# Performance work log

Hardware: AMD Instinct MI355X
Metric: run time of the kernel (lower is better)

## Reference

```python
import jax, jax.numpy as jnp
import numpy as np
import math

B, S, D, H = 2, 2048, 2048, 16
HD = D // H  # 128
EPS = 1e-5


def setup_inputs() -> dict:
    key = jax.random.key(0)
    ks = jax.random.split(key, 8)
    s = 0.02
    return {
        "x": jax.random.normal(ks[0], (B, S, D), jnp.float32),
        "ln1_s": jnp.ones((D,), jnp.float32),
        "ln1_b": jnp.zeros((D,), jnp.float32),
        "Wq": jax.random.normal(ks[1], (D, D), jnp.float32) * s,
        "Wk": jax.random.normal(ks[2], (D, D), jnp.float32) * s,
        "Wv": jax.random.normal(ks[3], (D, D), jnp.float32) * s,
        "Wo": jax.random.normal(ks[4], (D, D), jnp.float32) * s,
        "bo": jnp.zeros((D,), jnp.float32),
        "ln2_s": jnp.ones((D,), jnp.float32),
        "ln2_b": jnp.zeros((D,), jnp.float32),
        "W1": jax.random.normal(ks[5], (D, 4 * D), jnp.float32) * s,
        "b1": jnp.zeros((4 * D,), jnp.float32),
        "W2": jax.random.normal(ks[6], (4 * D, D), jnp.float32) * s,
        "b2": jnp.zeros((D,), jnp.float32),
    }


def _layernorm(x, scale, shift):
    mean = jnp.mean(x, axis=-1, keepdims=True)
    var = jnp.var(x, axis=-1, keepdims=True)  # unbiased=False
    return scale * (x - mean) * jax.lax.rsqrt(var + EPS) + shift


def _gelu_tanh(x):
    c = math.sqrt(2.0 / math.pi)
    return 0.5 * x * (1.0 + jnp.tanh(c * (x + 0.044715 * x * x * x)))


def reference(x, ln1_s, ln1_b, Wq, Wk, Wv, Wo, bo, ln2_s, ln2_b, W1, b1, W2, b2):
    b, n, d = x.shape
    # --- pre-norm MHA ---
    xn = _layernorm(x, ln1_s, ln1_b)
    q = (xn @ Wq).reshape(b, n, H, HD)
    k = (xn @ Wk).reshape(b, n, H, HD)
    v = (xn @ Wv).reshape(b, n, H, HD)
    scores = jnp.einsum("bqhd,bkhd->bhqk", q, k) / math.sqrt(HD)
    causal = jnp.tril(jnp.ones((n, n), bool))  # True = keep
    scores = jnp.where(causal, scores, -jnp.inf)
    attn = jax.nn.softmax(scores, axis=-1)
    ctx = jnp.einsum("bhqk,bkhd->bqhd", attn, v).reshape(b, n, d)
    attn_out = ctx @ Wo + bo
    x = x + attn_out
    # --- pre-norm FFN ---
    xn2 = _layernorm(x, ln2_s, ln2_b)
    h = _gelu_tanh(xn2 @ W1 + b1)
    ff_out = h @ W2 + b2
    return x + ff_out
```

## Files before the change

kernel.cpp:

```cpp
#include <hip/hip_runtime.h>

typedef unsigned short u16;
typedef __attribute__((ext_vector_type(8))) short short8;
typedef __attribute__((ext_vector_type(8))) __bf16 bf16x8;
typedef __attribute__((ext_vector_type(4))) float f32x4;

#define DEV __device__ __forceinline__
#define SB() __builtin_amdgcn_sched_barrier(0)

DEV float bf2f(u16 u) {
    union { unsigned v; float f; } x; x.v = ((unsigned)u) << 16; return x.f;
}
DEV u16 f2bf(float f) {
    union { float f; unsigned v; } x; x.f = f;
    unsigned r = x.v + 0x7fff + ((x.v >> 16) & 1);
    return (u16)(r >> 16);
}

DEV f32x4 mfma16(short8 a, short8 b, f32x4 c) {
    return __builtin_amdgcn_mfma_f32_16x16x32_bf16(
        __builtin_bit_cast(bf16x8, a), __builtin_bit_cast(bf16x8, b), c, 0, 0, 0);
}

typedef const __attribute__((address_space(1))) void* gas_ptr;
typedef __attribute__((address_space(3))) void* las_ptr;

__global__ __launch_bounds__(256) void transpose4_kernel(
    const float* __restrict__ w0, const float* __restrict__ w1,
    const float* __restrict__ w2, const float* __restrict__ w3,
    u16* __restrict__ out)
{
    __shared__ u16 t[64][65];
    int tid = threadIdx.x, z = blockIdx.z;
    const float* in = (z == 0) ? w0 : (z == 1) ? w1 : (z == 2) ? w2 : w3;
    u16* op0 = out + (size_t)z * 4194304ULL;
    int bc = blockIdx.x * 64, br = blockIdx.y * 64;
    int r = tid >> 2, cs = (tid & 3) * 16;
    const float* ip = in + (size_t)(br + r) * 2048 + bc + cs;
    f32x4 v0 = *(const f32x4*)ip, v1 = *(const f32x4*)(ip + 4),
          v2 = *(const f32x4*)(ip + 8), v3 = *(const f32x4*)(ip + 12);
#pragma unroll
    for (int j = 0; j < 4; j++) {
        t[r][cs + j]      = f2bf(v0[j]);
        t[r][cs + 4 + j]  = f2bf(v1[j]);
        t[r][cs + 8 + j]  = f2bf(v2[j]);
        t[r][cs + 12 + j] = f2bf(v3[j]);
    }
    __syncthreads();
    int n = tid >> 2, ks = (tid & 3) * 16;
    short8 o0, o1;
#pragma unroll
    for (int j = 0; j < 8; j++) { o0[j] = (short)t[ks + j][n]; o1[j] = (short)t[ks + 8 + j][n]; }
    u16* op = op0 + (size_t)(bc + n) * 2048 + br + ks;
    *(short8*)op = o0;
    *(short8*)(op + 8) = o1;
}

__global__ __launch_bounds__(256) void transpose_kernel(
    const float* __restrict__ in, u16* __restrict__ out, int R, int C)
{
    __shared__ u16 t[64][65];
    int tid = threadIdx.x;
    int bc = blockIdx.x * 64, br = blockIdx.y * 64;
    int r = tid >> 2, cs = (tid & 3) * 16;
    const float* ip = in + (size_t)(br + r) * C + bc + cs;
    f32x4 v0 = *(const f32x4*)ip, v1 = *(const f32x4*)(ip + 4),
          v2 = *(const f32x4*)(ip + 8), v3 = *(const f32x4*)(ip + 12);
#pragma unroll
    for (int j = 0; j < 4; j++) {
        t[r][cs + j]      = f2bf(v0[j]);
        t[r][cs + 4 + j]  = f2bf(v1[j]);
        t[r][cs + 8 + j]  = f2bf(v2[j]);
        t[r][cs + 12 + j] = f2bf(v3[j]);
    }
    __syncthreads();
    int n = tid >> 2, ks = (tid & 3) * 16;
    short8 o0, o1;
#pragma unroll
    for (int j = 0; j < 8; j++) { o0[j] = (short)t[ks + j][n]; o1[j] = (short)t[ks + 8 + j][n]; }
    u16* op = out + (size_t)(bc + n) * R + br + ks;
    *(short8*)op = o0;
    *(short8*)(op + 8) = o1;
}

template<int INBF>
__global__ __launch_bounds__(256) void ln_kernel(
    const void* __restrict__ xp, const float* __restrict__ sc, const float* __restrict__ sh,
    u16* __restrict__ out)
{
    int row = blockIdx.x, tid = threadIdx.x;
    float f[8], sum = 0.f, ss = 0.f;
    if (INBF) {
        short8 v = *(const short8*)((const u16*)xp + (size_t)row * 2048 + tid * 8);
#pragma unroll
        for (int j = 0; j < 8; j++) f[j] = bf2f((u16)v[j]);
    } else {
        const f32x4* xr = (const f32x4*)((const float*)xp + (size_t)row * 2048 + tid * 8);
        f32x4 a = xr[0], b = xr[1];
#pragma unroll
        for (int j = 0; j < 4; j++) { f[j] = a[j]; f[4 + j] = b[j]; }
    }
#pragma unroll
    for (int j = 0; j < 8; j++) { sum += f[j]; ss += f[j] * f[j]; }
#pragma unroll
    for (int m = 1; m < 64; m <<= 1) { sum += __shfl_xor(sum, m, 64); ss += __shfl_xor(ss, m, 64); }
    __shared__ float red[8];
    int w = tid >> 6, l = tid & 63;
    if (l == 0) { red[w] = sum; red[4 + w] = ss; }
    __syncthreads();
    sum = red[0] + red[1] + red[2] + red[3];
    ss  = red[4] + red[5] + red[6] + red[7];
    float mean = sum * (1.f / 2048.f);
    float var  = ss * (1.f / 2048.f) - mean * mean;
    float rstd = rsqrtf(var + 1e-5f);
    const f32x4* sp = (const f32x4*)(sc + tid * 8);
    const f32x4* bp = (const f32x4*)(sh + tid * 8);
    f32x4 s0 = sp[0], s1 = sp[1], b0 = bp[0], b1 = bp[1];
    short8 o;
#pragma unroll
    for (int j = 0; j < 4; j++) {
        o[j]     = (short)f2bf((f[j] - mean) * rstd * s0[j] + b0[j]);
        o[4 + j] = (short)f2bf((f[4 + j] - mean) * rstd * s1[j] + b1[j]);
    }
    *(short8*)(out + (size_t)row * 2048 + tid * 8) = o;
}

template<int EPI, int OUTF, int RESBF, int SPLITM, int SHAREB>
__global__ __launch_bounds__(576, 1) void gemm_pc(
    const u16* __restrict__ A, const u16* __restrict__ BT, void* __restrict__ Cp,
    const float* __restrict__ bias, const void* __restrict__ res, int M, int N, int K)
{
    __shared__ u16 As[3][256 * 64];
    __shared__ u16 Bs[3][128 * 64];
    int tid = threadIdx.x, l = tid & 63, w = tid >> 6;

    int nbx = gridDim.x, nby = gridDim.y;
    int nwg = nbx * nby;
    int orig = blockIdx.y * nbx + blockIdx.x;
    int wg = (orig & 7) * (nwg >> 3) + (orig >> 3);
    int bx, by;
    if (SHAREB) { bx = wg / nby; by = wg % nby; }
    else        { by = wg / nbx; bx = wg % nbx; }

    int mbase = by * 256, nbase = bx * 128;
    const u16* Ag = A + (size_t)mbase * K;
    const u16* Bg = BT + (size_t)nbase * K;
    int NT = K >> 6;

    if (w == 8) {
        auto pstage = [&](int s, int tt) {
#pragma unroll
            for (int g = 0; g < 32; g++) {
                int c = g * 64 + l;
                int r = c >> 3, ch = (c & 7) ^ (r & 7);
                __builtin_amdgcn_global_load_lds(
                    (gas_ptr)(Ag + (size_t)r * K + tt * 64 + ch * 8),
                    (las_ptr)&As[s][g * 512], 16, 0, 0);
            }
#pragma unroll
            for (int g = 0; g < 16; g++) {
                int c = g * 64 + l;
                int r = c >> 3, ch = (c & 7) ^ (r & 7);
                __builtin_amdgcn_global_load_lds(
                    (gas_ptr)(Bg + (size_t)r * K + tt * 64 + ch * 8),
                    (las_ptr)&Bs[s][g * 512], 16, 0, 0);
            }
        };
        pstage(0, 0); pstage(1, 1);
        asm volatile("s_waitcnt vmcnt(48)" ::: "memory");
        SB();
        __builtin_amdgcn_s_barrier();
        SB();
        for (int t = 0; t < NT; ++t) {
            if (t + 2 < NT) pstage((t + 2) % 3, t + 2);
            if (t + 1 < NT) {
                if (t + 2 < NT) { asm volatile("s_waitcnt vmcnt(48)" ::: "memory"); }
                else            { asm volatile("s_waitcnt vmcnt(0)"  ::: "memory"); }
            }
            SB();
            __builtin_amdgcn_s_barrier();
            SB();
        }
        return;
    }

    int wm = w >> 1, wn = w & 1;
    f32x4 acc[4][4];
#pragma unroll
    for (int i = 0; i < 4; i++)
#pragma unroll
        for (int j = 0; j < 4; j++) acc[i][j] = (f32x4){0.f, 0.f, 0.f, 0.f};

    __builtin_amdgcn_s_barrier();
    SB();
    int slot = 0;
    for (int t = 0; t < NT; ++t) {
        const u16* Ab = &As[slot][0];
        const u16* Bb = &Bs[slot][0];
        short8 af[2][4], bfr[2][4];
#pragma unroll
        for (int ks = 0; ks < 2; ks++) {
            int c = ks * 4 + (l >> 4);
#pragma unroll
            for (int i = 0; i < 4; i++) {
                int ra = wm * 64 + i * 16 + (l & 15);
                af[ks][i] = *(const short8*)&Ab[ra * 64 + ((c ^ (ra & 7)) << 3)];
                int rb = wn * 64 + i * 16 + (l & 15);
                bfr[ks][i] = *(const short8*)&Bb[rb * 64 + ((c ^ (rb & 7)) << 3)];
            }
        }
        __builtin_amdgcn_s_setprio(1);
#pragma unroll
        for (int ks = 0; ks < 2; ks++)
#pragma unroll
            for (int mi = 0; mi < 4; mi++)
#pragma unroll
                for (int ni = 0; ni < 4; ni++)
                    acc[mi][ni] = mfma16(af[ks][mi], bfr[ks][ni], acc[mi][ni]);
        __builtin_amdgcn_s_setprio(0);
        SB();
        __builtin_amdgcn_s_barrier();
        SB();
        slot = (slot == 2) ? 0 : slot + 1;
    }

#pragma unroll
    for (int mi = 0; mi < 4; mi++) {
#pragma unroll
        for (int ni = 0; ni < 4; ni++) {
            int col = nbase + wn * 64 + ni * 16 + (l & 15);
            float bval = (EPI != 0) ? bias[col] : 0.f;
#pragma unroll
            for (int r = 0; r < 4; r++) {
                int row = mbase + wm * 64 + mi * 16 + (l >> 4) * 4 + r;
                float v = acc[mi][ni][r];
                if (EPI == 1) {
                    size_t ridx = (size_t)row * N + col;
                    float rv = RESBF ? bf2f(((const u16*)res)[ridx]) : ((const float*)res)[ridx];
                    v += bval + rv;
                }
                if (EPI == 2) {
                    v += bval;
                    float tt = tanhf(0.7978845608028654f * (v + 0.044715f * v * v * v));
                    v = 0.5f * v * (1.f + tt);
                }
                if (SPLITM == 1) {
                    ((u16*)Cp)[(size_t)(col >> 11) * 8388608ULL + (size_t)row * 2048 + (col & 2047)] = f2bf(v);
                } else if (SPLITM == 2) {
                    ((u16*)Cp)[(size_t)(col >> 11) * 4194304ULL + (size_t)row * 2048 + (col & 2047)] = f2bf(v);
                } else if (OUTF) {
                    ((float*)Cp)[(size_t)row * N + col] = v;
                } else {
                    ((u16*)Cp)[(size_t)row * N + col] = f2bf(v);
                }
            }
        }
    }
}

__global__ __launch_bounds__(256, 2) void attn_kernel(
    const u16* __restrict__ Q, const u16* __restrict__ Kp, const u16* __restrict__ VTg,
    u16* __restrict__ O)
{
    __shared__ u16 Ks[64 * 128];
    __shared__ u16 VT[128 * 64];
    __shared__ u16 Ps[4 * 2048];
    int tid = threadIdx.x, l = tid & 63, w = tid >> 6;
    int qtl = (int)gridDim.x - 1 - (int)blockIdx.x;
    int bh = blockIdx.y, b = bh >> 4, h = bh & 15;
    const float SCALE = 0.08838834764831845f;
    int qbase = qtl * 128;
    size_t bS = (size_t)b * 2048;
    const u16* vrow = VTg + (size_t)bh * 128 * 2048;

    short8 qf[2][4];
#pragma unroll
    for (int mg = 0; mg < 2; mg++) {
        int qrow = qbase + w * 32 + mg * 16 + (l & 15);
        const u16* qp = Q + (bS + qrow) * 2048 + h * 128 + (l >> 4) * 8;
#pragma unroll
        for (int ds = 0; ds < 4; ds++) qf[mg][ds] = *(const short8*)(qp + ds * 32);
    }
    float m_[2][4], l_[2][4];
    f32x4 o_[2][8];
#pragma unroll
    for (int mg = 0; mg < 2; mg++)
#pragma unroll
        for (int r = 0; r < 4; r++) { m_[mg][r] = -1e30f; l_[mg][r] = 0.f; }
#pragma unroll
    for (int mg = 0; mg < 2; mg++)
#pragma unroll
        for (int d = 0; d < 8; d++) o_[mg][d] = (f32x4){0.f, 0.f, 0.f, 0.f};

    int ktmax = 2 * qtl + 1;
    for (int kt = 0; kt <= ktmax; ++kt) {
        int kbase = kt * 64;
#pragma unroll
        for (int it = 0; it < 4; ++it) {
            int slot = it * 256 + tid;
            int key = slot >> 4, dseg = slot & 15;
            short8 kv = *(const short8*)(Kp + (bS + kbase + key) * 2048 + h * 128 + dseg * 8);
            int kidx = ((key * 256 + dseg * 16) ^ ((key & 7) << 4)) >> 1;
            *(short8*)&Ks[kidx] = kv;
            int d = slot >> 3, k8 = slot & 7;
            short8 vv = *(const short8*)(vrow + (size_t)d * 2048 + kbase + k8 * 8);
            int vidx = ((d * 128 + k8 * 16) ^ ((d & 7) << 4)) >> 1;
            *(short8*)&VT[vidx] = vv;
        }
        __syncthreads();

        f32x4 s[2][4];
#pragma unroll
        for (int mg = 0; mg < 2; mg++)
#pragma unroll
            for (int kg = 0; kg < 4; kg++) s[mg][kg] = (f32x4){0.f, 0.f, 0.f, 0.f};
        __builtin_amdgcn_s_setprio(1);
#pragma unroll
        for (int kg = 0; kg < 4; kg++) {
            int key0 = kg * 16 + (l & 15);
#pragma unroll
            for (int ds = 0; ds < 4; ds++) {
                int i0 = ((key0 * 256 + ds * 64 + (l >> 4) * 16) ^ ((key0 & 7) << 4)) >> 1;
                short8 kb = *(const short8*)&Ks[i0];
                s[0][kg] = mfma16(qf[0][ds], kb, s[0][kg]);
                s[1][kg] = mfma16(qf[1][ds], kb, s[1][kg]);
            }
        }
        __builtin_amdgcn_s_setprio(0);

        bool domask = (kbase + 63) > qbase;
        float alpha[2][4];
        u16* Pw = &Ps[w * 2048];
#pragma unroll
        for (int mg = 0; mg < 2; mg++) {
#pragma unroll
            for (int r = 0; r < 4; r++) {
                int qrow = qbase + w * 32 + mg * 16 + (l >> 4) * 4 + r;
                float aa[4];
#pragma unroll
                for (int kg = 0; kg < 4; kg++) {
                    float a = s[mg][kg][r] * SCALE;
                    if (domask && (kbase + kg * 16 + (l & 15)) > qrow) a = -1e30f;
                    aa[kg] = a;
                }
                float mx = fmaxf(fmaxf(aa[0], aa[1]), fmaxf(aa[2], aa[3]));
                mx = fmaxf(mx, __shfl_xor(mx, 1, 64));
                mx = fmaxf(mx, __shfl_xor(mx, 2, 64));
                mx = fmaxf(mx, __shfl_xor(mx, 4, 64));
                mx = fmaxf(mx, __shfl_xor(mx, 8, 64));
                float mn = fmaxf(m_[mg][r], mx);
                float al = __expf(m_[mg][r] - mn);
                m_[mg][r] = mn;
                float p[4], rs = 0.f;
#pragma unroll
                for (int kg = 0; kg < 4; kg++) { p[kg] = __expf(aa[kg] - mn); rs += p[kg]; }
                rs += __shfl_xor(rs, 1, 64);
                rs += __shfl_xor(rs, 2, 64);
                rs += __shfl_xor(rs, 4, 64);
                rs += __shfl_xor(rs, 8, 64);
                l_[mg][r] = l_[mg][r] * al + rs;
                alpha[mg][r] = al;
#pragma unroll
                for (int kg = 0; kg < 4; kg++) {
                    int col = kg * 16 + (l & 15);
                    int lp = ((l >> 4) * 4 + r) | (((col >> 3) & 3) << 4);
                    Pw[(mg * 2 + (col >> 5)) * 512 + lp * 8 + (col & 7)] = f2bf(p[kg]);
                }
            }
        }
#pragma unroll
        for (int mg = 0; mg < 2; mg++)
#pragma unroll
            for (int dblk = 0; dblk < 8; dblk++)
#pragma unroll
                for (int r = 0; r < 4; r++) o_[mg][dblk][r] *= alpha[mg][r];

        __builtin_amdgcn_s_setprio(1);
#pragma unroll
        for (int kk = 0; kk < 2; kk++) {
            short8 pa0 = *(const short8*)&Pw[(0 * 2 + kk) * 512 + l * 8];
            short8 pa1 = *(const short8*)&Pw[(1 * 2 + kk) * 512 + l * 8];
#pragma unroll
            for (int dblk = 0; dblk < 8; dblk++) {
                int d = dblk * 16 + (l & 15);
                int iv = ((d * 128 + kk * 64 + (l >> 4) * 16) ^ ((d & 7) << 4)) >> 1;
                short8 vb = *(const short8*)&VT[iv];
                o_[0][dblk] = mfma16(pa0, vb, o_[0][dblk]);
                o_[1][dblk] = mfma16(pa1, vb, o_[1][dblk]);
            }
        }
        __builtin_amdgcn_s_setprio(0);
        __syncthreads();
    }

#pragma unroll
    for (int mg = 0; mg < 2; mg++) {
#pragma unroll
        for (int dblk = 0; dblk < 8; dblk++) {
#pragma unroll
            for (int r = 0; r < 4; r++) {
                int qrow = qbase + w * 32 + mg * 16 + (l >> 4) * 4 + r;
                float v = o_[mg][dblk][r] / l_[mg][r];
                O[(bS + qrow) * 2048 + h * 128 + dblk * 16 + (l & 15)] = f2bf(v);
            }
        }
    }
}

extern "C" void kernel_launch(void* const* d_in, const int* in_sizes, int n_in,
                              void* d_out, int out_size, void* d_ws, size_t ws_size,
                              hipStream_t stream)
{
    const float* x    = (const float*)d_in[0];
    const float* ln1s = (const float*)d_in[1];
    const float* ln1b = (const float*)d_in[2];
    const float* Wq   = (const float*)d_in[3];
    const float* Wk   = (const float*)d_in[4];
    const float* Wv   = (const float*)d_in[5];
    const float* Wo   = (const float*)d_in[6];
    const float* bo   = (const float*)d_in[7];
    const float* ln2s = (const float*)d_in[8];
    const float* ln2b = (const float*)d_in[9];
    const float* W1   = (const float*)d_in[10];
    const float* b1   = (const float*)d_in[11];
    const float* W2   = (const float*)d_in[12];
    const float* b2   = (const float*)d_in[13];
    float* out = (float*)d_out;
    const size_t ACT = 8388608ULL;

    u16* ws16 = (u16*)d_ws;
    u16* xn   = ws16;
    u16* q    = ws16 + ACT;
    u16* k    = ws16 + 2 * ACT;
    u16* vT   = ws16 + 3 * ACT;
    u16* hbuf = ws16 + 2 * ACT;
    u16* wt   = ws16 + 6 * ACT;
    u16* x2   = q;
    (void)k;

    dim3 blk(256), blkp(576);
    transpose4_kernel<<<dim3(32, 32, 4), blk, 0, stream>>>(Wq, Wk, Wv, Wo, wt);
    ln_kernel<0><<<4096, blk, 0, stream>>>(x, ln1s, ln1b, xn);
    gemm_pc<0, 0, 0, 1, 1><<<dim3(32, 16), blkp, 0, stream>>>(xn, wt, q, nullptr, nullptr, 4096, 4096, 2048);
    gemm_pc<0, 0, 0, 2, 1><<<dim3(32, 8), blkp, 0, stream>>>(wt + ACT, xn, vT, nullptr, nullptr, 2048, 4096, 2048);
    attn_kernel<<<dim3(16, 32), blk, 0, stream>>>(q, k, vT, xn);
    gemm_pc<1, 0, 0, 0, 0><<<dim3(16, 16), blkp, 0, stream>>>(xn, wt + 3 * (ACT >> 1), x2, bo, x, 4096, 2048, 2048);
    transpose_kernel<<<dim3(128, 32), blk, 0, stream>>>(W1, wt, 2048, 8192);
    ln_kernel<1><<<4096, blk, 0, stream>>>(x2, ln2s, ln2b, xn);
    gemm_pc<2, 0, 0, 0, 1><<<dim3(64, 16), blkp, 0, stream>>>(xn, wt, hbuf, b1, nullptr, 4096, 8192, 2048);
    transpose_kernel<<<dim3(32, 128), blk, 0, stream>>>(W2, wt, 8192, 2048);
    gemm_pc<1, 1, 1, 0, 0><<<dim3(16, 16), blkp, 0, stream>>>(hbuf, wt, out, b2, x2, 4096, 2048, 8192);
}
```

Baseline: 619.0 us.

## Replace producer-warp GEMM with all-wave double-buffered GEMM and wider N tiles

Removes the dedicated producer wave and triple buffering; all eight waves now issue global-to-LDS loads into a double buffer, with __syncthreads per K step. The N tile becomes a template parameter, and 256-wide tiles are used for the QKV and FFN1 GEMMs to increase data reuse per workgroup. The intent is higher arithmetic intensity and simpler scheduling. The trade-off is less latency hiding, since only one stage is prefetched ahead, plus more accumulator registers and LDS for the wider tiles.

```diff
diff --git a/kernel.cpp b/kernel.cpp
--- a/kernel.cpp
+++ b/kernel.cpp
@@ -125,14 +125,17 @@
     *(short8*)(out + (size_t)row * 2048 + tid * 8) = o;
 }
 
-template<int EPI, int OUTF, int RESBF, int SPLITM, int SHAREB>
-__global__ __launch_bounds__(576, 1) void gemm_pc(
+template<int BN, int EPI, int OUTF, int RESBF, int SPLITM, int SHAREB>
+__global__ __launch_bounds__(512, 1) void gemm_big(
     const u16* __restrict__ A, const u16* __restrict__ BT, void* __restrict__ Cp,
     const float* __restrict__ bias, const void* __restrict__ res, int M, int N, int K)
 {
-    __shared__ u16 As[3][256 * 64];
-    __shared__ u16 Bs[3][128 * 64];
+    constexpr int NJ = BN / 32;
+    constexpr int BCH = BN / 64;
+    __shared__ u16 As[2][256 * 64];
+    __shared__ u16 Bs[2][BN * 64];
     int tid = threadIdx.x, l = tid & 63, w = tid >> 6;
+    int wm = w >> 1, wn = w & 1;
 
     int nbx = gridDim.x, nby = gridDim.y;
     int nwg = nbx * nby;
@@ -142,93 +145,72 @@
     if (SHAREB) { bx = wg / nby; by = wg % nby; }
     else        { by = wg / nbx; bx = wg % nbx; }
 
-    int mbase = by * 256, nbase = bx * 128;
+    int mbase = by * 256, nbase = bx * BN;
     const u16* Ag = A + (size_t)mbase * K;
     const u16* Bg = BT + (size_t)nbase * K;
     int NT = K >> 6;
 
-    if (w == 8) {
-        auto pstage = [&](int s, int tt) {
-#pragma unroll
-            for (int g = 0; g < 32; g++) {
-                int c = g * 64 + l;
-                int r = c >> 3, ch = (c & 7) ^ (r & 7);
-                __builtin_amdgcn_global_load_lds(
-                    (gas_ptr)(Ag + (size_t)r * K + tt * 64 + ch * 8),
-                    (las_ptr)&As[s][g * 512], 16, 0, 0);
-            }
-#pragma unroll
-            for (int g = 0; g < 16; g++) {
-                int c = g * 64 + l;
-                int r = c >> 3, ch = (c & 7) ^ (r & 7);
-                __builtin_amdgcn_global_load_lds(
-                    (gas_ptr)(Bg + (size_t)r * K + tt * 64 + ch * 8),
-                    (las_ptr)&Bs[s][g * 512], 16, 0, 0);
-            }
-        };
-        pstage(0, 0); pstage(1, 1);
-        asm volatile("s_waitcnt vmcnt(48)" ::: "memory");
-        SB();
-        __builtin_amdgcn_s_barrier();
-        SB();
-        for (int t = 0; t < NT; ++t) {
-            if (t + 2 < NT) pstage((t + 2) % 3, t + 2);
-            if (t + 1 < NT) {
-                if (t + 2 < NT) { asm volatile("s_waitcnt vmcnt(48)" ::: "memory"); }
-                else            { asm volatile("s_waitcnt vmcnt(0)"  ::: "memory"); }
-            }
-            SB();
-            __builtin_amdgcn_s_barrier();
-            SB();
-        }
-        return;
-    }
-
-    int wm = w >> 1, wn = w & 1;
-    f32x4 acc[4][4];
+    auto stage = [&](int buf, int t) {
+#pragma unroll
+        for (int g = 0; g < 4; g++) {
+            int ci = g * 512 + tid;
+            int r = ci >> 3, ch = (ci & 7) ^ (r & 7);
+            __builtin_amdgcn_global_load_lds(
+                (gas_ptr)(Ag + (size_t)r * K + t * 64 + ch * 8),
+                (las_ptr)&As[buf][(g * 512 + w * 64) * 8], 16, 0, 0);
+        }
+#pragma unroll
+        for (int g = 0; g < BCH; g++) {
+            int ci = g * 512 + tid;
+            int r = ci >> 3, ch = (ci & 7) ^ (r & 7);
+            __builtin_amdgcn_global_load_lds(
+                (gas_ptr)(Bg + (size_t)r * K + t * 64 + ch * 8),
+                (las_ptr)&Bs[buf][(g * 512 + w * 64) * 8], 16, 0, 0);
+        }
+    };
+
+    f32x4 acc[4][NJ];
 #pragma unroll
     for (int i = 0; i < 4; i++)
 #pragma unroll
-        for (int j = 0; j < 4; j++) acc[i][j] = (f32x4){0.f, 0.f, 0.f, 0.f};
-
-    __builtin_amdgcn_s_barrier();
-    SB();
-    int slot = 0;
+        for (int j = 0; j < NJ; j++) acc[i][j] = (f32x4){0.f, 0.f, 0.f, 0.f};
+
+    stage(0, 0);
+    __syncthreads();
+    int buf = 0;
     for (int t = 0; t < NT; ++t) {
-        const u16* Ab = &As[slot][0];
-        const u16* Bb = &Bs[slot][0];
-        short8 af[2][4], bfr[2][4];
+        if (t + 1 < NT) stage(buf ^ 1, t + 1);
 #pragma unroll
         for (int ks = 0; ks < 2; ks++) {
+            short8 af[4], bfr[NJ];
             int c = ks * 4 + (l >> 4);
 #pragma unroll
             for (int i = 0; i < 4; i++) {
                 int ra = wm * 64 + i * 16 + (l & 15);
-                af[ks][i] = *(const short8*)&Ab[ra * 64 + ((c ^ (ra & 7)) << 3)];
-                int rb = wn * 64 + i * 16 + (l & 15);
-                bfr[ks][i] = *(const short8*)&Bb[rb * 64 + ((c ^ (rb & 7)) << 3)];
-            }
-        }
-        __builtin_amdgcn_s_setprio(1);
-#pragma unroll
-        for (int ks = 0; ks < 2; ks++)
-#pragma unroll
-            for (int mi = 0; mi < 4; mi++)
-#pragma unroll
-                for (int ni = 0; ni < 4; ni++)
-                    acc[mi][ni] = mfma16(af[ks][mi], bfr[ks][ni], acc[mi][ni]);
-        __builtin_amdgcn_s_setprio(0);
-        SB();
-        __builtin_amdgcn_s_barrier();
-        SB();
-        slot = (slot == 2) ? 0 : slot + 1;
+                af[i] = *(const short8*)&As[buf][ra * 64 + ((c ^ (ra & 7)) << 3)];
+            }
+#pragma unroll
+            for (int j = 0; j < NJ; j++) {
+                int rb = wn * (BN / 2) + j * 16 + (l & 15);
+                bfr[j] = *(const short8*)&Bs[buf][rb * 64 + ((c ^ (rb & 7)) << 3)];
+            }
+            __builtin_amdgcn_s_setprio(1);
+#pragma unroll
+            for (int i = 0; i < 4; i++)
+#pragma unroll
+                for (int j = 0; j < NJ; j++)
+                    acc[i][j] = mfma16(af[i], bfr[j], acc[i][j]);
+            __builtin_amdgcn_s_setprio(0);
+        }
+        __syncthreads();
+        buf ^= 1;
     }
 
 #pragma unroll
     for (int mi = 0; mi < 4; mi++) {
 #pragma unroll
-        for (int ni = 0; ni < 4; ni++) {
-            int col = nbase + wn * 64 + ni * 16 + (l & 15);
+        for (int ni = 0; ni < NJ; ni++) {
+            int col = nbase + wn * (BN / 2) + ni * 16 + (l & 15);
             float bval = (EPI != 0) ? bias[col] : 0.f;
 #pragma unroll
             for (int r = 0; r < 4; r++) {
@@ -438,16 +420,16 @@
     u16* x2   = q;
     (void)k;
 
-    dim3 blk(256), blkp(576);
+    dim3 blk(256), blkg(512);
     transpose4_kernel<<<dim3(32, 32, 4), blk, 0, stream>>>(Wq, Wk, Wv, Wo, wt);
     ln_kernel<0><<<4096, blk, 0, stream>>>(x, ln1s, ln1b, xn);
-    gemm_pc<0, 0, 0, 1, 1><<<dim3(32, 16), blkp, 0, stream>>>(xn, wt, q, nullptr, nullptr, 4096, 4096, 2048);
-    gemm_pc<0, 0, 0, 2, 1><<<dim3(32, 8), blkp, 0, stream>>>(wt + ACT, xn, vT, nullptr, nullptr, 2048, 4096, 2048);
+    gemm_big<256, 0, 0, 0, 1, 1><<<dim3(16, 16), blkg, 0, stream>>>(xn, wt, q, nullptr, nullptr, 4096, 4096, 2048);
+    gemm_big<128, 0, 0, 0, 2, 1><<<dim3(32, 8), blkg, 0, stream>>>(wt + ACT, xn, vT, nullptr, nullptr, 2048, 4096, 2048);
     attn_kernel<<<dim3(16, 32), blk, 0, stream>>>(q, k, vT, xn);
-    gemm_pc<1, 0, 0, 0, 0><<<dim3(16, 16), blkp, 0, stream>>>(xn, wt + 3 * (ACT >> 1), x2, bo, x, 4096, 2048, 2048);
+    gemm_big<128, 1, 0, 0, 0, 0><<<dim3(16, 16), blkg, 0, stream>>>(xn, wt + 3 * (ACT >> 1), x2, bo, x, 4096, 2048, 2048);
     transpose_kernel<<<dim3(128, 32), blk, 0, stream>>>(W1, wt, 2048, 8192);
     ln_kernel<1><<<4096, blk, 0, stream>>>(x2, ln2s, ln2b, xn);
-    gemm_pc<2, 0, 0, 0, 1><<<dim3(64, 16), blkp, 0, stream>>>(xn, wt, hbuf, b1, nullptr, 4096, 8192, 2048);
+    gemm_big<256, 2, 0, 0, 0, 1><<<dim3(32, 16), blkg, 0, stream>>>(xn, wt, hbuf, b1, nullptr, 4096, 8192, 2048);
     transpose_kernel<<<dim3(32, 128), blk, 0, stream>>>(W2, wt, 8192, 2048);
-    gemm_pc<1, 1, 1, 0, 0><<<dim3(16, 16), blkp, 0, stream>>>(hbuf, wt, out, b2, x2, 4096, 2048, 8192);
-}
+    gemm_big<128, 1, 1, 1, 0, 0><<<dim3(16, 16), blkg, 0, stream>>>(hbuf, wt, out, b2, x2, 4096, 2048, 8192);
+}
```

After: 709.5 us. +14.6%, slower.

## Add 256x256-tile producer-consumer GEMM for QK and FFN1 projections

Applied to the files above, without the earlier changes.

Adds a new gemm_pc2 kernel with 256x256 output tiles. Eight compute waves each own a 64x128 sub-tile, and one dedicated wave streams A and B into double-buffered LDS using global_load_lds. The QK projection and the FFN up-projection now use it, which halves the grid size and doubles operand reuse per loaded tile. The cost is 128 KB of LDS, double buffering instead of triple, 128 accumulator floats per lane, and fewer workgroups, which may leave CUs idle or raise register pressure.

```diff
diff --git a/kernel.cpp b/kernel.cpp
--- a/kernel.cpp
+++ b/kernel.cpp
@@ -229,6 +229,135 @@
 #pragma unroll
         for (int ni = 0; ni < 4; ni++) {
             int col = nbase + wn * 64 + ni * 16 + (l & 15);
+            float bval = (EPI != 0) ? bias[col] : 0.f;
+#pragma unroll
+            for (int r = 0; r < 4; r++) {
+                int row = mbase + wm * 64 + mi * 16 + (l >> 4) * 4 + r;
+                float v = acc[mi][ni][r];
+                if (EPI == 1) {
+                    size_t ridx = (size_t)row * N + col;
+                    float rv = RESBF ? bf2f(((const u16*)res)[ridx]) : ((const float*)res)[ridx];
+                    v += bval + rv;
+                }
+                if (EPI == 2) {
+                    v += bval;
+                    float tt = tanhf(0.7978845608028654f * (v + 0.044715f * v * v * v));
+                    v = 0.5f * v * (1.f + tt);
+                }
+                if (SPLITM == 1) {
+                    ((u16*)Cp)[(size_t)(col >> 11) * 8388608ULL + (size_t)row * 2048 + (col & 2047)] = f2bf(v);
+                } else if (SPLITM == 2) {
+                    ((u16*)Cp)[(size_t)(col >> 11) * 4194304ULL + (size_t)row * 2048 + (col & 2047)] = f2bf(v);
+                } else if (OUTF) {
+                    ((float*)Cp)[(size_t)row * N + col] = v;
+                } else {
+                    ((u16*)Cp)[(size_t)row * N + col] = f2bf(v);
+                }
+            }
+        }
+    }
+}
+
+template<int EPI, int OUTF, int RESBF, int SPLITM, int SHAREB>
+__global__ __launch_bounds__(576, 1) void gemm_pc2(
+    const u16* __restrict__ A, const u16* __restrict__ BT, void* __restrict__ Cp,
+    const float* __restrict__ bias, const void* __restrict__ res, int M, int N, int K)
+{
+    __shared__ u16 As[2][256 * 64];
+    __shared__ u16 Bs[2][256 * 64];
+    int tid = threadIdx.x, l = tid & 63, w = tid >> 6;
+
+    int nbx = gridDim.x, nby = gridDim.y;
+    int nwg = nbx * nby;
+    int orig = blockIdx.y * nbx + blockIdx.x;
+    int wg = (orig & 7) * (nwg >> 3) + (orig >> 3);
+    int bx, by;
+    if (SHAREB) { bx = wg / nby; by = wg % nby; }
+    else        { by = wg / nbx; bx = wg % nbx; }
+
+    int mbase = by * 256, nbase = bx * 256;
+    const u16* Ag = A + (size_t)mbase * K;
+    const u16* Bg = BT + (size_t)nbase * K;
+    int NT = K >> 6;
+
+    if (w == 8) {
+        auto pstage = [&](int s, int tt) {
+#pragma unroll
+            for (int g = 0; g < 32; g++) {
+                int c = g * 64 + l;
+                int r = c >> 3, ch = (c & 7) ^ (r & 7);
+                __builtin_amdgcn_global_load_lds(
+                    (gas_ptr)(Ag + (size_t)r * K + tt * 64 + ch * 8),
+                    (las_ptr)&As[s][g * 512], 16, 0, 0);
+            }
+#pragma unroll
+            for (int g = 0; g < 32; g++) {
+                int c = g * 64 + l;
+                int r = c >> 3, ch = (c & 7) ^ (r & 7);
+                __builtin_amdgcn_global_load_lds(
+                    (gas_ptr)(Bg + (size_t)r * K + tt * 64 + ch * 8),
+                    (las_ptr)&Bs[s][g * 512], 16, 0, 0);
+            }
+        };
+        pstage(0, 0);
+        asm volatile("s_waitcnt vmcnt(0)" ::: "memory");
+        SB();
+        __builtin_amdgcn_s_barrier();
+        SB();
+        for (int t = 0; t < NT; ++t) {
+            if (t + 1 < NT) pstage((t + 1) & 1, t + 1);
+            asm volatile("s_waitcnt vmcnt(0)" ::: "memory");
+            SB();
+            __builtin_amdgcn_s_barrier();
+            SB();
+        }
+        return;
+    }
+
+    int wm = w >> 1, wn = w & 1;
+    f32x4 acc[4][8];
+#pragma unroll
+    for (int i = 0; i < 4; i++)
+#pragma unroll
+        for (int j = 0; j < 8; j++) acc[i][j] = (f32x4){0.f, 0.f, 0.f, 0.f};
+
+    __builtin_amdgcn_s_barrier();
+    SB();
+    for (int t = 0; t < NT; ++t) {
+        const u16* Ab = &As[t & 1][0];
+        const u16* Bb = &Bs[t & 1][0];
+#pragma unroll
+        for (int ks = 0; ks < 2; ks++) {
+            short8 af[4], bfr[8];
+            int c = ks * 4 + (l >> 4);
+#pragma unroll
+            for (int i = 0; i < 4; i++) {
+                int ra = wm * 64 + i * 16 + (l & 15);
+                af[i] = *(const short8*)&Ab[ra * 64 + ((c ^ (ra & 7)) << 3)];
+            }
+#pragma unroll
+            for (int j = 0; j < 8; j++) {
+                int rb = wn * 128 + j * 16 + (l & 15);
+                bfr[j] = *(const short8*)&Bb[rb * 64 + ((c ^ (rb & 7)) << 3)];
+            }
+            __builtin_amdgcn_s_setprio(1);
+#pragma unroll
+            for (int i = 0; i < 4; i++)
+#pragma unroll
+                for (int j = 0; j < 8; j++)
+                    acc[i][j] = mfma16(af[i], bfr[j], acc[i][j]);
+            __builtin_amdgcn_s_setprio(0);
+        }
+        SB();
+        __builtin_amdgcn_s_barrier();
+        SB();
+    }
+
+#pragma unroll
+    for (int mi = 0; mi < 4; mi++) {
+#pragma unroll
+        for (int ni = 0; ni < 8; ni++) {
+            int col = nbase + wn * 128 + ni * 16 + (l & 15);
             float bval = (EPI != 0) ? bias[col] : 0.f;
 #pragma unroll
             for (int r = 0; r < 4; r++) {
@@ -441,13 +570,13 @@
     dim3 blk(256), blkp(576);
     transpose4_kernel<<<dim3(32, 32, 4), blk, 0, stream>>>(Wq, Wk, Wv, Wo, wt);
     ln_kernel<0><<<4096, blk, 0, stream>>>(x, ln1s, ln1b, xn);
-    gemm_pc<0, 0, 0, 1, 1><<<dim3(32, 16), blkp, 0, stream>>>(xn, wt, q, nullptr, nullptr, 4096, 4096, 2048);
+    gemm_pc2<0, 0, 0, 1, 1><<<dim3(16, 16), blkp, 0, stream>>>(xn, wt, q, nullptr, nullptr, 4096, 4096, 2048);
     gemm_pc<0, 0, 0, 2, 1><<<dim3(32, 8), blkp, 0, stream>>>(wt + ACT, xn, vT, nullptr, nullptr, 2048, 4096, 2048);
     attn_kernel<<<dim3(16, 32), blk, 0, stream>>>(q, k, vT, xn);
     gemm_pc<1, 0, 0, 0, 0><<<dim3(16, 16), blkp, 0, stream>>>(xn, wt + 3 * (ACT >> 1), x2, bo, x, 4096, 2048, 2048);
     transpose_kernel<<<dim3(128, 32), blk, 0, stream>>>(W1, wt, 2048, 8192);
     ln_kernel<1><<<4096, blk, 0, stream>>>(x2, ln2s, ln2b, xn);
-    gemm_pc<2, 0, 0, 0, 1><<<dim3(64, 16), blkp, 0, stream>>>(xn, wt, hbuf, b1, nullptr, 4096, 8192, 2048);
+    gemm_pc2<2, 0, 0, 0, 1><<<dim3(32, 16), blkp, 0, stream>>>(xn, wt, hbuf, b1, nullptr, 4096, 8192, 2048);
     transpose_kernel<<<dim3(32, 128), blk, 0, stream>>>(W2, wt, 8192, 2048);
     gemm_pc<1, 1, 1, 0, 0><<<dim3(16, 16), blkp, 0, stream>>>(hbuf, wt, out, b2, x2, 4096, 2048, 8192);
 }
```

Result: slower. 1.051 ms (+69.8%).
